# Kernel optimization log

Measured on AMD Instinct MI355X. Metric: run time of the kernel, lower is better.

The kernel has to match this reference:

```python
import jax, jax.numpy as jnp
import numpy as np

B, LQ, LK, LKL = 4, 1024, 1024, 512
DX, H, DK = 1024, 16, 64
ALPHA = 0.5
NEG = -1e9
EPS = 1e-5


def setup_inputs() -> dict:
    key = jax.random.key(0)
    ks = jax.random.split(key, 24)
    s = 0.02
    inp = {
        "q": jax.random.normal(ks[0], (B, LQ, DX), jnp.float32),
        "k": jax.random.normal(ks[1], (B, LK, DX), jnp.float32),
        "v": jax.random.normal(ks[2], (B, LK, DX), jnp.float32),
        "kl": jax.random.normal(ks[3], (B, LKL, DX), jnp.float32),
        "vl": jax.random.normal(ks[4], (B, LKL, DX), jnp.float32),
        "pad_mask": jax.random.randint(ks[5], (B, LQ, LK), 0, 2).astype(bool),
        "pad_mask_l": jax.random.randint(ks[6], (B, LQ, LKL), 0, 2).astype(bool),
        "wq_w": jax.random.normal(ks[7], (DX, H * DK), jnp.float32) * s,
        "wq_b": jnp.zeros((H * DK,), jnp.float32),
        "wk_w": jax.random.normal(ks[8], (DX, H * DK), jnp.float32) * s,
        "wk_b": jnp.zeros((H * DK,), jnp.float32),
        "wv_w": jax.random.normal(ks[9], (DX, H * DK), jnp.float32) * s,
        "wv_b": jnp.zeros((H * DK,), jnp.float32),
        "wkl_w": jax.random.normal(ks[10], (DX, H * DK), jnp.float32) * s,
        "wkl_b": jnp.zeros((H * DK,), jnp.float32),
        "wvl_w": jax.random.normal(ks[11], (DX, H * DK), jnp.float32) * s,
        "wvl_b": jnp.zeros((H * DK,), jnp.float32),
        "wo_w": jax.random.normal(ks[12], (H * DK, DX), jnp.float32) * s,
        "wo_b": jnp.zeros((DX,), jnp.float32),
        "ln_g": jnp.ones((DX,), jnp.float32),
        "ln_b": jnp.zeros((DX,), jnp.float32),
    }
    return inp


def _heads(x, w, b, L):
    # (B, L, DX) @ (DX, H*DK) -> (B, H, L, DK)
    y = x @ w + b
    return y.reshape(B, L, H, DK).transpose(0, 2, 1, 3)


def _attn(qh, kh, vh, mask):
    # qh: (B,H,Lq,D), kh/vh: (B,H,Lk,D), mask: (B,Lq,Lk) bool (True = masked)
    scores = jnp.einsum("bhqd,bhkd->bhqk", qh, kh) / np.sqrt(DK).astype(np.float32)
    scores = jnp.where(mask[:, None, :, :], NEG, scores)
    attn = jax.nn.softmax(scores, axis=-1)
    out = jnp.einsum("bhqk,bhkd->bhqd", attn, vh)
    return out, attn


def reference(q, k, v, kl, vl, pad_mask, pad_mask_l,
              wq_w, wq_b, wk_w, wk_b, wv_w, wv_b,
              wkl_w, wkl_b, wvl_w, wvl_b, wo_w, wo_b, ln_g, ln_b):
    X = q
    qh = _heads(q, wq_w, wq_b, LQ)
    kh = _heads(k, wk_w, wk_b, LK)
    vh = _heads(v, wv_w, wv_b, LK)
    klh = _heads(kl, wkl_w, wkl_b, LKL)
    vlh = _heads(vl, wvl_w, wvl_b, LKL)

    out_c, attn_c = _attn(qh, kh, vh, pad_mask)
    out_l, attn_l = _attn(qh, klh, vlh, pad_mask_l)

    out = ALPHA * out_c + (1.0 - ALPHA) * out_l          # (B,H,Lq,DK)
    out = out.transpose(0, 2, 1, 3).reshape(B, LQ, H * DK)
    out = out @ wo_w + wo_b                              # dropout = identity (eval)
    y = out + X
    mu = jnp.mean(y, axis=-1, keepdims=True)
    var = jnp.var(y, axis=-1, keepdims=True)
    y = (y - mu) / jnp.sqrt(var + EPS) * ln_g + ln_b
    return y, attn_c, attn_l
```

## Files before the change

kernel.cpp:

```cpp
#include <hip/hip_runtime.h>
#include <hip/hip_bf16.h>

#define B_   4
#define LQ_  1024
#define LK_  1024
#define LKL_ 512
#define DX_  1024
#define H_   16
#define DK_  64
#define HDK_ 1024
#define NEG_ -1e9f
#define EPS_ 1e-5f

typedef __bf16 bf16_t;
typedef __bf16 bf16x8 __attribute__((ext_vector_type(8)));
typedef __bf16 bf16x4 __attribute__((ext_vector_type(4)));
typedef float  f32x4  __attribute__((ext_vector_type(4)));

__device__ inline f32x4 mfma16(bf16x8 a, bf16x8 b, f32x4 c) {
    return __builtin_amdgcn_mfma_f32_16x16x32_bf16(a, b, c, 0, 0, 0);
}

__device__ __forceinline__ void gload16(const void* g, void* l) {
    __builtin_amdgcn_global_load_lds(
        (const __attribute__((address_space(1))) void*)g,
        (__attribute__((address_space(3))) void*)l, 16, 0, 0);
}

__device__ inline float waveMax(float v) {
#pragma unroll
    for (int o = 32; o > 0; o >>= 1) v = fmaxf(v, __shfl_xor(v, o, 64));
    return v;
}
__device__ inline float waveSum(float v) {
#pragma unroll
    for (int o = 32; o > 0; o >>= 1) v += __shfl_xor(v, o, 64);
    return v;
}

template<int STRIDE>
__device__ inline int sidx(int row, int col) {
    return (row * STRIDE + col) ^ ((row & 15) << 3);
}

__global__ __launch_bounds__(256) void bitpack_mask_kernel(
    const void* __restrict__ mc, const void* __restrict__ ml,
    unsigned long long* __restrict__ bc, unsigned long long* __restrict__ bl)
{
    __shared__ unsigned fl[4];
    {
        const unsigned w = ((const unsigned*)mc)[threadIdx.x];
        const unsigned long long b01 = __ballot(w <= 1u);
        const unsigned long long bfl = __ballot(w == 0u || w == 0x3F800000u);
        if ((threadIdx.x & 63) == 0)
            fl[threadIdx.x >> 6] = ((b01 == ~0ull) ? 1u : 0u) | ((bfl == ~0ull) ? 2u : 0u);
    }
    __syncthreads();
    const unsigned comb = fl[0] & fl[1] & fl[2] & fl[3];
    const unsigned flag = (comb & 1u) ? 0u : ((comb & 2u) ? 2u : 1u);

    const size_t NC = (size_t)B_ * LQ_ * LK_;
    const int lane = threadIdx.x & 63;
    const size_t g = (size_t)blockIdx.x * 256 + threadIdx.x;
    const bool inC = g < NC;
    const size_t idx = inC ? g : g - NC;
    const void* src = inC ? mc : ml;
    bool m;
    if (flag == 0u)      m = ((const int*)src)[idx] != 0;
    else if (flag == 2u) m = ((const float*)src)[idx] != 0.0f;
    else                 m = ((const unsigned char*)src)[idx] != 0;
    const unsigned long long bal = __ballot(m);
    if (lane == 0) {
        unsigned long long* dst = inC ? bc : bl;
        dst[idx >> 6] = bal;
    }
}

struct WtArgs {
    const float* W[6];
    bf16_t* Wt[6];
};
__global__ __launch_bounds__(256) void wtrans_all_kernel(WtArgs a)
{
    __shared__ float T[64][65];
    const int z = blockIdx.z;
    const float* W = a.W[z];
    bf16_t* Wt = a.Wt[z];
    const int k0 = blockIdx.y * 64, n0 = blockIdx.x * 64;
    const int t = threadIdx.x;
    const int lr = t >> 2, c0 = (t & 3) * 16;
#pragma unroll
    for (int j = 0; j < 4; ++j) {
        const float4 v = *(const float4*)&W[(size_t)(k0 + lr) * DX_ + n0 + c0 + j * 4];
        T[lr][c0 + j * 4 + 0] = v.x; T[lr][c0 + j * 4 + 1] = v.y;
        T[lr][c0 + j * 4 + 2] = v.z; T[lr][c0 + j * 4 + 3] = v.w;
    }
    __syncthreads();
    const int dr = t >> 2;
    bf16x8 o0, o1;
#pragma unroll
    for (int j = 0; j < 8; ++j) {
        o0[j] = (bf16_t)T[c0 + j][dr];
        o1[j] = (bf16_t)T[c0 + 8 + j][dr];
    }
    *(bf16x8*)&Wt[(size_t)(n0 + dr) * DX_ + k0 + c0]     = o0;
    *(bf16x8*)&Wt[(size_t)(n0 + dr) * DX_ + k0 + c0 + 8] = o1;
}

struct TvArgs {
    const bf16_t* V[2];
    bf16_t* Vt[2];
    int L[2];
    int xt[2];
};
__global__ __launch_bounds__(256) void transpose_v_all_kernel(TvArgs a)
{
    __shared__ bf16_t T[64][72];
    const int z = blockIdx.z;
    if ((int)blockIdx.x >= a.xt[z]) return;
    const int L = a.L[z];
    const int bh = blockIdx.y, l0 = blockIdx.x * 64;
    const bf16_t* Vb = a.V[z] + (size_t)bh * L * 64;
    bf16_t* Vtb = a.Vt[z] + (size_t)bh * 64 * L;
    const int t = threadIdx.x;
    {
        const int lr = t >> 2, dc = (t & 3) * 16;
        const bf16x8 x = *(const bf16x8*)&Vb[(size_t)(l0 + lr) * 64 + dc];
        const bf16x8 y = *(const bf16x8*)&Vb[(size_t)(l0 + lr) * 64 + dc + 8];
#pragma unroll
        for (int j = 0; j < 8; ++j) { T[lr][dc + j] = x[j]; T[lr][dc + 8 + j] = y[j]; }
    }
    __syncthreads();
    {
        const int dr = t >> 2, lc = (t & 3) * 16;
        bf16x8 o0, o1;
#pragma unroll
        for (int j = 0; j < 8; ++j) { o0[j] = T[lc + j][dr]; o1[j] = T[lc + 8 + j][dr]; }
        *(bf16x8*)&Vtb[(size_t)dr * L + l0 + lc]     = o0;
        *(bf16x8*)&Vtb[(size_t)dr * L + l0 + lc + 8] = o1;
    }
}

template<int MODE>
__device__ __forceinline__ void gemm2_body(
    const void* __restrict__ Avoid, const bf16_t* __restrict__ Bt,
    const float* __restrict__ bias,
    void* __restrict__ out, const float* __restrict__ resid, int lshift,
    bf16_t* __restrict__ As, bf16_t* __restrict__ Bs)
{
    char* const AsB = (char*)As;
    char* const BsB = (char*)Bs;
    const int tid = threadIdx.x, wave = tid >> 6, lane = tid & 63;
    const int m0 = blockIdx.y * 128, n0 = blockIdx.x * 128;
    const int wr4 = (wave >> 1) * 32, wc2 = (wave & 1) * 64;

    f32x4 acc[2][4] = {};

    const int srow = wave * 8 + (lane >> 3);
    const int sslot = lane & 7;

    for (int k0 = 0; k0 < 1024; k0 += 64) {
        __syncthreads();
#pragma unroll
        for (int j = 0; j < 2; ++j) {
            const int row = srow + j * 64;
            const int gs = sslot ^ (row & 7);
            if (MODE == 0) {
                const float* Af = (const float*)Avoid;
                const float4* srcp = (const float4*)&Af[(size_t)(m0 + row) * 1024 + k0 + gs * 8];
                const float4 xa = srcp[0], xb = srcp[1];
                bf16x8 t;
                t[0] = (bf16_t)xa.x; t[1] = (bf16_t)xa.y; t[2] = (bf16_t)xa.z; t[3] = (bf16_t)xa.w;
                t[4] = (bf16_t)xb.x; t[5] = (bf16_t)xb.y; t[6] = (bf16_t)xb.z; t[7] = (bf16_t)xb.w;
                *(bf16x8*)(AsB + j * 8192 + wave * 1024 + lane * 16) = t;
            } else {
                const bf16_t* Ab = (const bf16_t*)Avoid;
                gload16(&Ab[(size_t)(m0 + row) * 1024 + k0 + gs * 8],
                        AsB + j * 8192 + wave * 1024);
            }
            gload16(&Bt[(size_t)(n0 + row) * 1024 + k0 + gs * 8],
                    BsB + j * 8192 + wave * 1024);
        }
        __syncthreads();
#pragma unroll
        for (int kk = 0; kk < 2; ++kk) {
            bf16x8 av[2], bv[4];
#pragma unroll
            for (int i = 0; i < 2; ++i) {
                const int r = wr4 + i * 16 + (lane & 15);
                av[i] = *(const bf16x8*)(AsB + r * 128 + (((kk * 4 + (lane >> 4)) ^ (r & 7)) * 16));
            }
#pragma unroll
            for (int n = 0; n < 4; ++n) {
                const int r = wc2 + n * 16 + (lane & 15);
                bv[n] = *(const bf16x8*)(BsB + r * 128 + (((kk * 4 + (lane >> 4)) ^ (r & 7)) * 16));
            }
#pragma unroll
            for (int i = 0; i < 2; ++i)
#pragma unroll
                for (int n = 0; n < 4; ++n)
                    acc[i][n] = mfma16(av[i], bv[n], acc[i][n]);
        }
    }

#pragma unroll
    for (int i = 0; i < 2; ++i) {
#pragma unroll
        for (int n = 0; n < 4; ++n) {
            const int col = n0 + wc2 + n * 16 + (lane & 15);
            const float bs = bias[col];
            const int row0 = m0 + wr4 + i * 16 + (lane >> 4) * 4;
            if (MODE == 0) {
                const int b = row0 >> lshift, l = row0 & ((1 << lshift) - 1);
                const int h = col >> 6, d = col & 63;
#pragma unroll
                for (int r = 0; r < 4; ++r)
                    ((bf16_t*)out)[(((size_t)(b * H_ + h) << lshift) + l + r) * DK_ + d] =
                        (bf16_t)(acc[i][n][r] + bs);
            } else {
#pragma unroll
                for (int r = 0; r < 4; ++r) {
                    const size_t idx = (size_t)(row0 + r) * DX_ + col;
                    ((float*)out)[idx] = acc[i][n][r] + bs + resid[idx];
                }
            }
        }
    }
}

struct ProjArgs {
    const float* A[5];
    const bf16_t* Bt[5];
    const float* bias[5];
    bf16_t* out[5];
    int mt[5];
    int lshift[5];
};
__global__ __launch_bounds__(512, 2) void proj_gemm_kernel(ProjArgs a)
{
    __shared__ bf16_t As[128 * 64];
    __shared__ bf16_t Bs[128 * 64];
    const int z = blockIdx.z;
    if ((int)blockIdx.y >= a.mt[z]) return;
    gemm2_body<0>(a.A[z], a.Bt[z], a.bias[z], a.out[z], nullptr, a.lshift[z], As, Bs);
}

__global__ __launch_bounds__(512, 2) void out_gemm_kernel(
    const bf16_t* __restrict__ A, const bf16_t* __restrict__ Bt,
    const float* __restrict__ bias, float* __restrict__ out,
    const float* __restrict__ resid)
{
    __shared__ bf16_t As[128 * 64];
    __shared__ bf16_t Bs[128 * 64];
    gemm2_body<2>(A, Bt, bias, out, resid, 0, As, Bs);
}

template<int LKX, bool COMBINE>
__device__ __forceinline__ void fused_branch_body(
    const bf16_t* __restrict__ Qh, const bf16_t* __restrict__ Kh,
    const bf16_t* __restrict__ Vt, const unsigned* __restrict__ bits,
    float* __restrict__ S, bf16_t* __restrict__ comb, bf16_t* __restrict__ Ssh)
{
    const int sid = (blockIdx.x & 7) * 512 + (blockIdx.x >> 3);
    const int bh = sid >> 6, qt = sid & 63;
    const int b = bh >> 4, h = bh & 15;
    const int q0 = qt * 16;
    const int wave = threadIdx.x >> 6, lane = threadIdx.x & 63;
    const int lr = lane & 15, lk8 = (lane >> 4) * 8;
    constexpr int WORDS = LKX / 32;
    constexpr int WPS   = LKX / 128;

    const bf16_t* Qb  = Qh + (size_t)bh * LQ_ * DK_;
    const bf16_t* Kb  = Kh + (size_t)bh * LKX * DK_;
    const bf16_t* Vtb = Vt + (size_t)bh * DK_ * LKX;
    float* Sout = S + (size_t)bh * LQ_ * LKX;

    const int pwi = wave * WPS + (lane >> 4);
    const size_t prow_base = (size_t)(b * LQ_ + q0 + (lane & 15)) * WORDS;
    const unsigned w0 = bits[prow_base + pwi];
    unsigned w1 = 0;
    if (WPS == 8) w1 = bits[prow_base + pwi + 4];

    bf16x8 qf[2];
#pragma unroll
    for (int ks = 0; ks < 2; ++ks)
        qf[ks] = *(const bf16x8*)&Qb[(size_t)(q0 + lr) * DK_ + ks * 32 + lk8];

    constexpr int KTS = LKX / 64;
#pragma unroll
    for (int kt = 0; kt < KTS; ++kt) {
        const int kbase = wave * (LKX / 4) + kt * 16;
        const bf16x8 b0 = *(const bf16x8*)&Kb[(size_t)(kbase + lr) * DK_ + lk8];
        const bf16x8 b1 = *(const bf16x8*)&Kb[(size_t)(kbase + lr) * DK_ + 32 + lk8];
        f32x4 acc = {};
        acc = mfma16(qf[0], b0, acc);
        acc = mfma16(qf[1], b1, acc);
        const int d = kt >> 1;
        const int sh = (kbase & 16) + (lane & 15);
#pragma unroll
        for (int r = 0; r < 4; ++r) {
            const int row = (lane >> 4) * 4 + r;
            const int srcl = row + ((d & 3) << 4);
            const unsigned word = __shfl((WPS == 8 && d >= 4) ? w1 : w0, srcl, 64);
            const bool msk = (word >> sh) & 1u;
            Ssh[sidx<LKX>(row, kbase + (lane & 15))] = (bf16_t)(msk ? NEG_ : acc[r] * 0.125f);
        }
    }
    __syncthreads();

    constexpr int NP8 = LKX / 512;
#pragma unroll 2
    for (int i = 0; i < 4; ++i) {
        const int row = wave * 4 + i;
        float p[NP8 * 8];
        float m = -INFINITY;
#pragma unroll
        for (int ps = 0; ps < NP8; ++ps) {
            const bf16x8 sv = *(const bf16x8*)&Ssh[sidx<LKX>(row, ps * 512 + lane * 8)];
#pragma unroll
            for (int j = 0; j < 8; ++j) {
                p[ps * 8 + j] = (float)sv[j];
                m = fmaxf(m, p[ps * 8 + j]);
            }
        }
        m = waveMax(m);
        float s = 0.f;
#pragma unroll
        for (int j = 0; j < NP8 * 8; ++j) { p[j] = __expf(p[j] - m); s += p[j]; }
        s = waveSum(s);
        const float inv = 1.f / s;
#pragma unroll
        for (int ps = 0; ps < NP8; ++ps) {
            const int col = ps * 512 + lane * 8;
            bf16x8 pb;
#pragma unroll
            for (int j = 0; j < 8; ++j) pb[j] = (bf16_t)(p[ps * 8 + j] * inv);
            *(bf16x8*)&Ssh[sidx<LKX>(row, col)] = pb;
        }
    }
    __syncthreads();

    f32x4 acc_o = {};
    const int d0 = wave * 16;
#pragma unroll
    for (int ks = 0; ks < LKX / 32; ++ks) {
        const bf16x8 bb = *(const bf16x8*)&Vtb[(size_t)(d0 + lr) * LKX + ks * 32 + lk8];
        const bf16x8 a  = *(const bf16x8*)&Ssh[sidx<LKX>(lr, ks * 32 + lk8)];
        acc_o = mfma16(a, bb, acc_o);
    }

#pragma unroll
    for (int r = 0; r < 4; ++r) {
        const int row = q0 + (lane >> 4) * 4 + r;
        const size_t idx = ((size_t)b * LQ_ + row) * HDK_ + h * DK_ + d0 + (lane & 15);
        const float half = 0.5f * acc_o[r];
        if (COMBINE) comb[idx] = (bf16_t)((float)comb[idx] + half);
        else         comb[idx] = (bf16_t)half;
    }

#pragma unroll
    for (int i = 0; i < 4; ++i) {
        const int row = wave * 4 + i;
        const int rowg = q0 + row;
#pragma unroll
        for (int ps = 0; ps < NP8; ++ps) {
            const int col = ps * 512 + lane * 8;
            const bf16x8 pv8 = *(const bf16x8*)&Ssh[sidx<LKX>(row, col)];
            f32x4 o0, o1;
#pragma unroll
            for (int j = 0; j < 4; ++j) { o0[j] = (float)pv8[j]; o1[j] = (float)pv8[4 + j]; }
            __builtin_nontemporal_store(o0, (f32x4*)&Sout[(size_t)rowg * LKX + col]);
            __builtin_nontemporal_store(o1, (f32x4*)&Sout[(size_t)rowg * LKX + col + 4]);
        }
    }
}

__global__ __launch_bounds__(256, 5) void fused_c_kernel(
    const bf16_t* __restrict__ Qh, const bf16_t* __restrict__ Kh,
    const bf16_t* __restrict__ Vt, const unsigned* __restrict__ bits,
    float* __restrict__ S, bf16_t* __restrict__ comb)
{
    __shared__ bf16_t Ssh[16 * LK_];
    fused_branch_body<LK_, false>(Qh, Kh, Vt, bits, S, comb, Ssh);
}

__global__ __launch_bounds__(256, 5) void fused_l_kernel(
    const bf16_t* __restrict__ Qh, const bf16_t* __restrict__ Kh,
    const bf16_t* __restrict__ Vt, const unsigned* __restrict__ bits,
    float* __restrict__ S, bf16_t* __restrict__ comb)
{
    __shared__ bf16_t Ssh[16 * LKL_];
    fused_branch_body<LKL_, true>(Qh, Kh, Vt, bits, S, comb, Ssh);
}

__global__ __launch_bounds__(256) void ln_kernel(
    const float* __restrict__ Y, const float* __restrict__ g,
    const float* __restrict__ be, float* __restrict__ out)
{
    __shared__ float red1[4], red2[4];
    const int tid = threadIdx.x, wave = tid >> 6, lane = tid & 63;
    const float* p = Y + (size_t)blockIdx.x * DX_;
    const float4 x = *(const float4*)&p[tid * 4];
    float s  = x.x + x.y + x.z + x.w;
    float ss = x.x * x.x + x.y * x.y + x.z * x.z + x.w * x.w;
    s = waveSum(s); ss = waveSum(ss);
    if (lane == 0) { red1[wave] = s; red2[wave] = ss; }
    __syncthreads();
    s  = red1[0] + red1[1] + red1[2] + red1[3];
    ss = red2[0] + red2[1] + red2[2] + red2[3];
    const float mean = s * (1.f / DX_);
    const float var  = ss * (1.f / DX_) - mean * mean;
    const float rstd = rsqrtf(var + EPS_);
    const float4 gg = *(const float4*)&g[tid * 4];
    const float4 bb = *(const float4*)&be[tid * 4];
    float4 o;
    o.x = (x.x - mean) * rstd * gg.x + bb.x;
    o.y = (x.y - mean) * rstd * gg.y + bb.y;
    o.z = (x.z - mean) * rstd * gg.z + bb.z;
    o.w = (x.w - mean) * rstd * gg.w + bb.w;
    *(float4*)&out[(size_t)blockIdx.x * DX_ + tid * 4] = o;
}

extern "C" void kernel_launch(void* const* d_in, const int* in_sizes, int n_in,
                              void* d_out, int out_size, void* d_ws, size_t ws_size,
                              hipStream_t stream)
{
    const float* q    = (const float*)d_in[0];
    const float* k    = (const float*)d_in[1];
    const float* v    = (const float*)d_in[2];
    const float* kl   = (const float*)d_in[3];
    const float* vl   = (const float*)d_in[4];
    const void*  mask  = d_in[5];
    const void*  maskl = d_in[6];
    const float* wq_w  = (const float*)d_in[7];
    const float* wq_b  = (const float*)d_in[8];
    const float* wk_w  = (const float*)d_in[9];
    const float* wk_b  = (const float*)d_in[10];
    const float* wv_w  = (const float*)d_in[11];
    const float* wv_b  = (const float*)d_in[12];
    const float* wkl_w = (const float*)d_in[13];
    const float* wkl_b = (const float*)d_in[14];
    const float* wvl_w = (const float*)d_in[15];
    const float* wvl_b = (const float*)d_in[16];
    const float* wo_w  = (const float*)d_in[17];
    const float* wo_b  = (const float*)d_in[18];
    const float* ln_g  = (const float*)d_in[19];
    const float* ln_b  = (const float*)d_in[20];

    char* ws = (char*)d_ws;
    const size_t MiB = 1u << 20;
    float*  ypre = (float*) (ws);
    bf16_t* qh   = (bf16_t*)(ws +  32 * MiB);
    bf16_t* kh   = (bf16_t*)(ws +  40 * MiB);
    bf16_t* klh  = (bf16_t*)(ws +  48 * MiB);
    bf16_t* vh   = (bf16_t*)(ws +  52 * MiB);
    bf16_t* vlh  = (bf16_t*)(ws +  60 * MiB);
    bf16_t* vt   = (bf16_t*)(ws +  64 * MiB);
    bf16_t* vlt  = (bf16_t*)(ws +  72 * MiB);
    bf16_t* wqT  = (bf16_t*)(ws +  76 * MiB);
    bf16_t* wkT  = (bf16_t*)(ws +  78 * MiB);
    bf16_t* wvT  = (bf16_t*)(ws +  80 * MiB);
    bf16_t* wklT = (bf16_t*)(ws +  82 * MiB);
    bf16_t* wvlT = (bf16_t*)(ws +  84 * MiB);
    bf16_t* woT  = (bf16_t*)(ws +  86 * MiB);
    unsigned long long* bitc = (unsigned long long*)(ws + 89 * MiB);
    unsigned long long* bitl = (unsigned long long*)(ws + 89 * MiB + 512 * 1024);
    bf16_t* comb = (bf16_t*)(ws + 90 * MiB);

    float* y_out = (float*)d_out;
    float* Sc = y_out + (size_t)B_ * LQ_ * DX_;
    float* Sl = Sc + (size_t)B_ * H_ * LQ_ * LK_;

    bitpack_mask_kernel<<<dim3((B_*LQ_*(LK_+LKL_)) / 256), 256, 0, stream>>>(
        mask, maskl, bitc, bitl);

    {
        WtArgs a;
        a.W[0] = wq_w;  a.Wt[0] = wqT;
        a.W[1] = wk_w;  a.Wt[1] = wkT;
        a.W[2] = wv_w;  a.Wt[2] = wvT;
        a.W[3] = wkl_w; a.Wt[3] = wklT;
        a.W[4] = wvl_w; a.Wt[4] = wvlT;
        a.W[5] = wo_w;  a.Wt[5] = woT;
        wtrans_all_kernel<<<dim3(16, 16, 6), 256, 0, stream>>>(a);
    }

    {
        ProjArgs a;
        a.A[0] = q;  a.Bt[0] = wqT;  a.bias[0] = wq_b;  a.out[0] = qh;  a.mt[0] = 32; a.lshift[0] = 10;
        a.A[1] = k;  a.Bt[1] = wkT;  a.bias[1] = wk_b;  a.out[1] = kh;  a.mt[1] = 32; a.lshift[1] = 10;
        a.A[2] = kl; a.Bt[2] = wklT; a.bias[2] = wkl_b; a.out[2] = klh; a.mt[2] = 16; a.lshift[2] = 9;
        a.A[3] = v;  a.Bt[3] = wvT;  a.bias[3] = wv_b;  a.out[3] = vh;  a.mt[3] = 32; a.lshift[3] = 10;
        a.A[4] = vl; a.Bt[4] = wvlT; a.bias[4] = wvl_b; a.out[4] = vlh; a.mt[4] = 16; a.lshift[4] = 9;
        proj_gemm_kernel<<<dim3(8, 32, 5), 512, 0, stream>>>(a);
    }

    {
        TvArgs a;
        a.V[0] = vh;  a.Vt[0] = vt;  a.L[0] = LK_;  a.xt[0] = 16;
        a.V[1] = vlh; a.Vt[1] = vlt; a.L[1] = LKL_; a.xt[1] = 8;
        transpose_v_all_kernel<<<dim3(16, 64, 2), 256, 0, stream>>>(a);
    }

    fused_c_kernel<<<dim3(4096), 256, 0, stream>>>(qh, kh,  vt,  (const unsigned*)bitc, Sc, comb);
    fused_l_kernel<<<dim3(4096), 256, 0, stream>>>(qh, klh, vlt, (const unsigned*)bitl, Sl, comb);

    out_gemm_kernel<<<dim3(8, 32), 512, 0, stream>>>(comb, woT, wo_b, ypre, q);

    ln_kernel<<<4096, 256, 0, stream>>>(ypre, ln_g, ln_b, y_out);
}
```

Baseline: 383.0 us.

## Merge both attention branches into one launch and sum partial outputs in out GEMM

The two attention kernels are combined into a single 8192-block launch that dispatches on block index to the full or the local-key branch. Each branch writes its half-weighted output to a separate buffer, which removes the read-modify-write dependency between them. The output GEMM now loads both buffers and adds them while staging A into LDS, giving up its async global-to-LDS loads for that operand. Score stores also switch from nontemporal to ordinary stores, which may affect cache behaviour on the large attention-matrix writes.

```diff
diff --git a/kernel.cpp b/kernel.cpp
--- a/kernel.cpp
+++ b/kernel.cpp
@@ -143,7 +143,8 @@
 
 template<int MODE>
 __device__ __forceinline__ void gemm2_body(
-    const void* __restrict__ Avoid, const bf16_t* __restrict__ Bt,
+    const void* __restrict__ Avoid, const bf16_t* __restrict__ A2,
+    const bf16_t* __restrict__ Bt,
     const float* __restrict__ bias,
     void* __restrict__ out, const float* __restrict__ resid, int lshift,
     bf16_t* __restrict__ As, bf16_t* __restrict__ Bs)
@@ -174,9 +175,14 @@
                 t[4] = (bf16_t)xb.x; t[5] = (bf16_t)xb.y; t[6] = (bf16_t)xb.z; t[7] = (bf16_t)xb.w;
                 *(bf16x8*)(AsB + j * 8192 + wave * 1024 + lane * 16) = t;
             } else {
-                const bf16_t* Ab = (const bf16_t*)Avoid;
-                gload16(&Ab[(size_t)(m0 + row) * 1024 + k0 + gs * 8],
-                        AsB + j * 8192 + wave * 1024);
+                const bf16_t* Ac = (const bf16_t*)Avoid;
+                const bf16x8 xa = *(const bf16x8*)&Ac[(size_t)(m0 + row) * 1024 + k0 + gs * 8];
+                const bf16x8 xb = *(const bf16x8*)&A2[(size_t)(m0 + row) * 1024 + k0 + gs * 8];
+                bf16x8 t;
+#pragma unroll
+                for (int jj = 0; jj < 8; ++jj)
+                    t[jj] = (bf16_t)((float)xa[jj] + (float)xb[jj]);
+                *(bf16x8*)(AsB + j * 8192 + wave * 1024 + lane * 16) = t;
             }
             gload16(&Bt[(size_t)(n0 + row) * 1024 + k0 + gs * 8],
                     BsB + j * 8192 + wave * 1024);
@@ -242,26 +248,27 @@
     __shared__ bf16_t Bs[128 * 64];
     const int z = blockIdx.z;
     if ((int)blockIdx.y >= a.mt[z]) return;
-    gemm2_body<0>(a.A[z], a.Bt[z], a.bias[z], a.out[z], nullptr, a.lshift[z], As, Bs);
+    gemm2_body<0>(a.A[z], nullptr, a.Bt[z], a.bias[z], a.out[z], nullptr, a.lshift[z], As, Bs);
 }
 
 __global__ __launch_bounds__(512, 2) void out_gemm_kernel(
-    const bf16_t* __restrict__ A, const bf16_t* __restrict__ Bt,
+    const bf16_t* __restrict__ Ac, const bf16_t* __restrict__ Al,
+    const bf16_t* __restrict__ Bt,
     const float* __restrict__ bias, float* __restrict__ out,
     const float* __restrict__ resid)
 {
     __shared__ bf16_t As[128 * 64];
     __shared__ bf16_t Bs[128 * 64];
-    gemm2_body<2>(A, Bt, bias, out, resid, 0, As, Bs);
-}
-
-template<int LKX, bool COMBINE>
+    gemm2_body<2>(Ac, Al, Bt, bias, out, resid, 0, As, Bs);
+}
+
+template<int LKX>
 __device__ __forceinline__ void fused_branch_body(
     const bf16_t* __restrict__ Qh, const bf16_t* __restrict__ Kh,
     const bf16_t* __restrict__ Vt, const unsigned* __restrict__ bits,
-    float* __restrict__ S, bf16_t* __restrict__ comb, bf16_t* __restrict__ Ssh)
-{
-    const int sid = (blockIdx.x & 7) * 512 + (blockIdx.x >> 3);
+    float* __restrict__ S, bf16_t* __restrict__ comb,
+    bf16_t* __restrict__ Ssh, int sid)
+{
     const int bh = sid >> 6, qt = sid & 63;
     const int b = bh >> 4, h = bh & 15;
     const int q0 = qt * 16;
@@ -353,9 +360,7 @@
     for (int r = 0; r < 4; ++r) {
         const int row = q0 + (lane >> 4) * 4 + r;
         const size_t idx = ((size_t)b * LQ_ + row) * HDK_ + h * DK_ + d0 + (lane & 15);
-        const float half = 0.5f * acc_o[r];
-        if (COMBINE) comb[idx] = (bf16_t)((float)comb[idx] + half);
-        else         comb[idx] = (bf16_t)half;
+        comb[idx] = (bf16_t)(0.5f * acc_o[r]);
     }
 
 #pragma unroll
@@ -369,28 +374,29 @@
             f32x4 o0, o1;
 #pragma unroll
             for (int j = 0; j < 4; ++j) { o0[j] = (float)pv8[j]; o1[j] = (float)pv8[4 + j]; }
-            __builtin_nontemporal_store(o0, (f32x4*)&Sout[(size_t)rowg * LKX + col]);
-            __builtin_nontemporal_store(o1, (f32x4*)&Sout[(size_t)rowg * LKX + col + 4]);
-        }
-    }
-}
-
-__global__ __launch_bounds__(256, 5) void fused_c_kernel(
+            *(f32x4*)&Sout[(size_t)rowg * LKX + col]     = o0;
+            *(f32x4*)&Sout[(size_t)rowg * LKX + col + 4] = o1;
+        }
+    }
+}
+
+__global__ __launch_bounds__(256, 5) void fused_attn_all_kernel(
     const bf16_t* __restrict__ Qh, const bf16_t* __restrict__ Kh,
-    const bf16_t* __restrict__ Vt, const unsigned* __restrict__ bits,
-    float* __restrict__ S, bf16_t* __restrict__ comb)
+    const bf16_t* __restrict__ Klh,
+    const bf16_t* __restrict__ Vt, const bf16_t* __restrict__ Vlt,
+    const unsigned* __restrict__ bitc, const unsigned* __restrict__ bitl,
+    float* __restrict__ Sc, float* __restrict__ Sl,
+    bf16_t* __restrict__ comb_c, bf16_t* __restrict__ comb_l)
 {
     __shared__ bf16_t Ssh[16 * LK_];
-    fused_branch_body<LK_, false>(Qh, Kh, Vt, bits, S, comb, Ssh);
-}
-
-__global__ __launch_bounds__(256, 5) void fused_l_kernel(
-    const bf16_t* __restrict__ Qh, const bf16_t* __restrict__ Kh,
-    const bf16_t* __restrict__ Vt, const unsigned* __restrict__ bits,
-    float* __restrict__ S, bf16_t* __restrict__ comb)
-{
-    __shared__ bf16_t Ssh[16 * LKL_];
-    fused_branch_body<LKL_, true>(Qh, Kh, Vt, bits, S, comb, Ssh);
+    const int bid = blockIdx.x;
+    const int xcd = bid & 7;
+    const int seq = bid >> 3;
+    if (seq < 512) {
+        fused_branch_body<LK_ >(Qh, Kh,  Vt,  bitc, Sc, comb_c, Ssh, xcd * 512 + seq);
+    } else {
+        fused_branch_body<LKL_>(Qh, Klh, Vlt, bitl, Sl, comb_l, Ssh, xcd * 512 + (seq - 512));
+    }
 }
 
 __global__ __launch_bounds__(256) void ln_kernel(
@@ -465,7 +471,8 @@
     bf16_t* woT  = (bf16_t*)(ws +  86 * MiB);
     unsigned long long* bitc = (unsigned long long*)(ws + 89 * MiB);
     unsigned long long* bitl = (unsigned long long*)(ws + 89 * MiB + 512 * 1024);
-    bf16_t* comb = (bf16_t*)(ws + 90 * MiB);
+    bf16_t* comb_c = (bf16_t*)(ws +  90 * MiB);
+    bf16_t* comb_l = (bf16_t*)(ws +  98 * MiB);
 
     float* y_out = (float*)d_out;
     float* Sc = y_out + (size_t)B_ * LQ_ * DX_;
@@ -502,10 +509,12 @@
         transpose_v_all_kernel<<<dim3(16, 64, 2), 256, 0, stream>>>(a);
     }
 
-    fused_c_kernel<<<dim3(4096), 256, 0, stream>>>(qh, kh,  vt,  (const unsigned*)bitc, Sc, comb);
-    fused_l_kernel<<<dim3(4096), 256, 0, stream>>>(qh, klh, vlt, (const unsigned*)bitl, Sl, comb);
-
-    out_gemm_kernel<<<dim3(8, 32), 512, 0, stream>>>(comb, woT, wo_b, ypre, q);
+    fused_attn_all_kernel<<<dim3(8192), 256, 0, stream>>>(
+        qh, kh, klh, vt, vlt,
+        (const unsigned*)bitc, (const unsigned*)bitl,
+        Sc, Sl, comb_c, comb_l);
+
+    out_gemm_kernel<<<dim3(8, 32), 512, 0, stream>>>(comb_c, comb_l, woT, wo_b, ypre, q);
 
     ln_kernel<<<4096, 256, 0, stream>>>(ypre, ln_g, ln_b, y_out);
 }
```

Result: slower. 403.0 us (+5.2%).
